# Optimization experiments

Hardware: AMD Instinct MI355X
Metric: run time of the kernel (lower is better)

## Reference

```python
import jax, jax.numpy as jnp
import numpy as np

B, S, DIN, DOUT = 4, 2048, 4096, 4096
W_SCALE = 64.0   # makes round(weight*scale) produce non-trivial int8 values
X_SCALE = 16.0   # input_scale so x*scale truncates to non-zero int32 values


def setup_inputs() -> dict:
    key = jax.random.key(0)
    k1, k2, k3 = jax.random.split(key, 3)
    # kaiming_uniform fan_in: bound = sqrt(6/fan_in)
    bound = float(np.sqrt(6.0 / DIN))
    weight = jax.random.uniform(k1, (DOUT, DIN), jnp.float32, -bound, bound)
    x = jax.random.normal(k2, (B, S, DIN), jnp.float32)
    bias = jax.random.normal(k3, (DOUT,), jnp.float32) * 0.01
    weight_scale = jnp.full((DOUT,), W_SCALE, jnp.float32)
    input_scale = jnp.full((1,), X_SCALE, jnp.float32)
    return {"x": x, "weight": weight, "bias": bias,
            "weight_scale": weight_scale, "input_scale": input_scale}


def reference(x, weight, bias, weight_scale, input_scale):
    # x = x * input_scale (pre-scale path of forward)
    xs = x * input_scale
    # fake-quant weights: round to int8 with wraparound, like torch .to(int8)
    w_int = jnp.round(weight * weight_scale[:, None]).astype(jnp.int8)
    # x.to(torch.int32): truncation toward zero
    x_int = xs.astype(jnp.int32)
    # F.linear on the integer-valued tensors (computed in f32: values are exact ints)
    acc = jnp.einsum('bsd,od->bso', x_int.astype(jnp.float32),
                     w_int.astype(jnp.float32))
    acc = acc + bias  # bias added inside linear
    # dequant: divide by per-channel weight_scale and the scalar input_scale
    out = acc / (weight_scale * input_scale)
    return out
```

## Files before the change

kernel.cpp:

```cpp
#include <hip/hip_runtime.h>

#define GM 8192
#define GN 4096
#define GK 4096

#define BM 128
#define BN 256
#define BK 64

using int4v = __attribute__((ext_vector_type(4))) int;

__global__ __launch_bounds__(256) void quant_x_k(const float4* __restrict__ x,
                                                 unsigned int* __restrict__ xq,
                                                 const float* __restrict__ iscale,
                                                 int n4) {
    int i = blockIdx.x * blockDim.x + threadIdx.x;
    if (i >= n4) return;
    float s = *iscale;
    float4 v = x[i];
    int q0 = (int)(v.x * s);
    int q1 = (int)(v.y * s);
    int q2 = (int)(v.z * s);
    int q3 = (int)(v.w * s);
    unsigned int packed = (unsigned int)(q0 & 0xff)
                        | ((unsigned int)(q1 & 0xff) << 8)
                        | ((unsigned int)(q2 & 0xff) << 16)
                        | ((unsigned int)(q3 & 0xff) << 24);
    xq[i] = packed;
}

__global__ __launch_bounds__(256) void quant_w_k(const float4* __restrict__ w,
                                                 unsigned int* __restrict__ wq,
                                                 const float* __restrict__ wscale,
                                                 int n4) {
    int i = blockIdx.x * blockDim.x + threadIdx.x;
    if (i >= n4) return;
    int row = i >> 10;
    float s = wscale[row];
    float4 v = w[i];
    int q0 = (int)rintf(v.x * s);
    int q1 = (int)rintf(v.y * s);
    int q2 = (int)rintf(v.z * s);
    int q3 = (int)rintf(v.w * s);
    unsigned int packed = (unsigned int)(q0 & 0xff)
                        | ((unsigned int)(q1 & 0xff) << 8)
                        | ((unsigned int)(q2 & 0xff) << 16)
                        | ((unsigned int)(q3 & 0xff) << 24);
    wq[i] = packed;
}

__global__ __launch_bounds__(256, 2) void qlinear_gemm_i8(
    const signed char* __restrict__ Aq,
    const signed char* __restrict__ Bq,
    const float* __restrict__ bias,
    const float* __restrict__ wscale,
    const float* __restrict__ iscale,
    float* __restrict__ C) {
    __shared__ signed char As[BM * BK];
    __shared__ signed char Bs[BN * BK];

    const int tid  = threadIdx.x;
    const int wave = tid >> 6;
    const int lane = tid & 63;
    const int m0 = blockIdx.x * BM;
    const int n0 = blockIdx.y * BN;
    const int wm = (wave >> 1) * 64;
    const int wn = (wave & 1) * 128;

    int4v acc[4][8];
#pragma unroll
    for (int i = 0; i < 4; ++i)
#pragma unroll
        for (int j = 0; j < 8; ++j)
            acc[i][j] = int4v{0, 0, 0, 0};

    const int kcl = (((lane & 3) ^ ((lane >> 3) & 3))) * 16;

    const int segA = wave * 2;
    const signed char* gA0 = Aq + (size_t)(m0 + segA * 16 + (lane >> 2)) * GK + kcl;
    signed char* lA0 = As + segA * 1024 + lane * 16;
    const int segB = wave * 4;
    const signed char* gB0 = Bq + (size_t)(n0 + segB * 16 + (lane >> 2)) * GK + kcl;
    signed char* lB0 = Bs + segB * 1024 + lane * 16;

    const int pos = ((lane >> 4) ^ ((lane >> 1) & 3)) * 16;
    const signed char* fA = As + (wm + (lane & 15)) * BK + pos;
    const signed char* fB = Bs + (wn + (lane & 15)) * BK + pos;

#define GLL16(g, l)                                                     \
    __builtin_amdgcn_global_load_lds(                                   \
        (__attribute__((address_space(1))) void*)(void*)(g),            \
        (__attribute__((address_space(3))) void*)(l), 16, 0, 0)

    for (int k0 = 0; k0 < GK; k0 += BK) {
        GLL16(gA0 + k0, lA0);
        GLL16(gA0 + (size_t)16 * GK + k0, lA0 + 1024);
        GLL16(gB0 + k0, lB0);
        GLL16(gB0 + (size_t)16 * GK + k0, lB0 + 1024);
        GLL16(gB0 + (size_t)32 * GK + k0, lB0 + 2048);
        GLL16(gB0 + (size_t)48 * GK + k0, lB0 + 3072);
        __syncthreads();

        int4v a[4], b[8];
#pragma unroll
        for (int i = 0; i < 4; ++i)
            a[i] = *(const int4v*)(fA + i * 16 * BK);
#pragma unroll
        for (int j = 0; j < 8; ++j)
            b[j] = *(const int4v*)(fB + j * 16 * BK);
#pragma unroll
        for (int mi = 0; mi < 4; ++mi)
#pragma unroll
            for (int ni = 0; ni < 8; ++ni)
                acc[mi][ni] = __builtin_amdgcn_mfma_i32_16x16x64_i8(
                    a[mi], b[ni], acc[mi][ni], 0, 0, 0);
        __syncthreads();
    }

    const float isc = *iscale;
#pragma unroll
    for (int ni = 0; ni < 8; ++ni) {
        const int col = n0 + wn + ni * 16 + (lane & 15);
        const float bs = bias[col];
        const float inv = 1.0f / (wscale[col] * isc);
#pragma unroll
        for (int mi = 0; mi < 4; ++mi) {
            const int row0 = m0 + wm + mi * 16 + (lane >> 4) * 4;
#pragma unroll
            for (int r = 0; r < 4; ++r) {
                C[(size_t)(row0 + r) * GN + col] =
                    ((float)acc[mi][ni][r] + bs) * inv;
            }
        }
    }
#undef GLL16
}

extern "C" void kernel_launch(void* const* d_in, const int* in_sizes, int n_in,
                              void* d_out, int out_size, void* d_ws, size_t ws_size,
                              hipStream_t stream) {
    const float* x      = (const float*)d_in[0];
    const float* w      = (const float*)d_in[1];
    const float* bias   = (const float*)d_in[2];
    const float* wscale = (const float*)d_in[3];
    const float* iscale = (const float*)d_in[4];
    float* out = (float*)d_out;

    signed char* xq = (signed char*)d_ws;
    signed char* wq = xq + (size_t)GM * GK;

    const int n4x = GM * GK / 4;
    quant_x_k<<<n4x / 256, 256, 0, stream>>>((const float4*)x,
                                             (unsigned int*)xq, iscale, n4x);
    const int n4w = GN * GK / 4;
    quant_w_k<<<n4w / 256, 256, 0, stream>>>((const float4*)w,
                                             (unsigned int*)wq, wscale, n4w);

    dim3 grid(GM / BM, GN / BN);
    qlinear_gemm_i8<<<grid, 256, 0, stream>>>(xq, wq, bias, wscale, iscale, out);
}
```

Measured before the change: 404.4 us.

## Double-buffer LDS tiles in int8 GEMM and fuse quantization kernels

The GEMM main loop now keeps two LDS buffers. It issues the global-to-LDS loads for the next K tile before running the MFMAs on the current one, so load latency can overlap compute instead of stalling at a barrier each iteration. The two quantization kernels are merged into one launch, and each thread now handles 16 elements with 16-byte stores. The trade-off is double the LDS use per block (48 KB), which could limit occupancy.

```diff
diff --git a/kernel.cpp b/kernel.cpp
--- a/kernel.cpp
+++ b/kernel.cpp
@@ -10,43 +10,43 @@
 
 using int4v = __attribute__((ext_vector_type(4))) int;
 
-__global__ __launch_bounds__(256) void quant_x_k(const float4* __restrict__ x,
-                                                 unsigned int* __restrict__ xq,
-                                                 const float* __restrict__ iscale,
-                                                 int n4) {
-    int i = blockIdx.x * blockDim.x + threadIdx.x;
-    if (i >= n4) return;
-    float s = *iscale;
-    float4 v = x[i];
-    int q0 = (int)(v.x * s);
-    int q1 = (int)(v.y * s);
-    int q2 = (int)(v.z * s);
-    int q3 = (int)(v.w * s);
-    unsigned int packed = (unsigned int)(q0 & 0xff)
-                        | ((unsigned int)(q1 & 0xff) << 8)
-                        | ((unsigned int)(q2 & 0xff) << 16)
-                        | ((unsigned int)(q3 & 0xff) << 24);
-    xq[i] = packed;
-}
-
-__global__ __launch_bounds__(256) void quant_w_k(const float4* __restrict__ w,
-                                                 unsigned int* __restrict__ wq,
-                                                 const float* __restrict__ wscale,
-                                                 int n4) {
-    int i = blockIdx.x * blockDim.x + threadIdx.x;
-    if (i >= n4) return;
-    int row = i >> 10;
-    float s = wscale[row];
-    float4 v = w[i];
-    int q0 = (int)rintf(v.x * s);
-    int q1 = (int)rintf(v.y * s);
-    int q2 = (int)rintf(v.z * s);
-    int q3 = (int)rintf(v.w * s);
-    unsigned int packed = (unsigned int)(q0 & 0xff)
-                        | ((unsigned int)(q1 & 0xff) << 8)
-                        | ((unsigned int)(q2 & 0xff) << 16)
-                        | ((unsigned int)(q3 & 0xff) << 24);
-    wq[i] = packed;
+__global__ __launch_bounds__(256) void quant_both(
+    const float4* __restrict__ x, uint4* __restrict__ xq,
+    const float4* __restrict__ w, uint4* __restrict__ wq,
+    const float* __restrict__ wscale, const float* __restrict__ iscale) {
+    const int b = blockIdx.x;
+    if (b < 8192) {
+        const float s = *iscale;
+        const int i = b * 256 + threadIdx.x;
+        unsigned int q[4];
+#pragma unroll
+        for (int j = 0; j < 4; ++j) {
+            float4 v = x[i * 4 + j];
+            int q0 = (int)(v.x * s);
+            int q1 = (int)(v.y * s);
+            int q2 = (int)(v.z * s);
+            int q3 = (int)(v.w * s);
+            q[j] = (unsigned int)(q0 & 0xff) | ((unsigned int)(q1 & 0xff) << 8)
+                 | ((unsigned int)(q2 & 0xff) << 16) | ((unsigned int)(q3 & 0xff) << 24);
+        }
+        xq[i] = uint4{q[0], q[1], q[2], q[3]};
+    } else {
+        const int row = b - 8192;
+        const float s = wscale[row];
+        const int i = row * 256 + threadIdx.x;
+        unsigned int q[4];
+#pragma unroll
+        for (int j = 0; j < 4; ++j) {
+            float4 v = w[i * 4 + j];
+            int q0 = (int)rintf(v.x * s);
+            int q1 = (int)rintf(v.y * s);
+            int q2 = (int)rintf(v.z * s);
+            int q3 = (int)rintf(v.w * s);
+            q[j] = (unsigned int)(q0 & 0xff) | ((unsigned int)(q1 & 0xff) << 8)
+                 | ((unsigned int)(q2 & 0xff) << 16) | ((unsigned int)(q3 & 0xff) << 24);
+        }
+        wq[i] = uint4{q[0], q[1], q[2], q[3]};
+    }
 }
 
 __global__ __launch_bounds__(256, 2) void qlinear_gemm_i8(
@@ -56,8 +56,8 @@
     const float* __restrict__ wscale,
     const float* __restrict__ iscale,
     float* __restrict__ C) {
-    __shared__ signed char As[BM * BK];
-    __shared__ signed char Bs[BN * BK];
+    __shared__ signed char As[2][BM * BK];
+    __shared__ signed char Bs[2][BN * BK];
 
     const int tid  = threadIdx.x;
     const int wave = tid >> 6;
@@ -74,33 +74,43 @@
         for (int j = 0; j < 8; ++j)
             acc[i][j] = int4v{0, 0, 0, 0};
 
-    const int kcl = (((lane & 3) ^ ((lane >> 3) & 3))) * 16;
-
+    const int kcl = ((lane & 3) ^ ((lane >> 3) & 3)) * 16;
     const int segA = wave * 2;
-    const signed char* gA0 = Aq + (size_t)(m0 + segA * 16 + (lane >> 2)) * GK + kcl;
-    signed char* lA0 = As + segA * 1024 + lane * 16;
+    const signed char* gA = Aq + (size_t)(m0 + segA * 16 + (lane >> 2)) * GK + kcl;
+    const int ldsA = segA * 1024 + lane * 16;
     const int segB = wave * 4;
-    const signed char* gB0 = Bq + (size_t)(n0 + segB * 16 + (lane >> 2)) * GK + kcl;
-    signed char* lB0 = Bs + segB * 1024 + lane * 16;
+    const signed char* gB = Bq + (size_t)(n0 + segB * 16 + (lane >> 2)) * GK + kcl;
+    const int ldsB = segB * 1024 + lane * 16;
 
     const int pos = ((lane >> 4) ^ ((lane >> 1) & 3)) * 16;
-    const signed char* fA = As + (wm + (lane & 15)) * BK + pos;
-    const signed char* fB = Bs + (wn + (lane & 15)) * BK + pos;
+    const int fAo = (wm + (lane & 15)) * BK + pos;
+    const int fBo = (wn + (lane & 15)) * BK + pos;
 
 #define GLL16(g, l)                                                     \
     __builtin_amdgcn_global_load_lds(                                   \
         (__attribute__((address_space(1))) void*)(void*)(g),            \
         (__attribute__((address_space(3))) void*)(l), 16, 0, 0)
 
+#define STAGE(buf, k)                                                   \
+    do {                                                                \
+        GLL16(gA + (k), &As[buf][ldsA]);                                \
+        GLL16(gA + (size_t)16 * GK + (k), &As[buf][ldsA + 1024]);       \
+        GLL16(gB + (k), &Bs[buf][ldsB]);                                \
+        GLL16(gB + (size_t)16 * GK + (k), &Bs[buf][ldsB + 1024]);       \
+        GLL16(gB + (size_t)32 * GK + (k), &Bs[buf][ldsB + 2048]);       \
+        GLL16(gB + (size_t)48 * GK + (k), &Bs[buf][ldsB + 3072]);       \
+    } while (0)
+
+    STAGE(0, 0);
+    __syncthreads();
+
     for (int k0 = 0; k0 < GK; k0 += BK) {
-        GLL16(gA0 + k0, lA0);
-        GLL16(gA0 + (size_t)16 * GK + k0, lA0 + 1024);
-        GLL16(gB0 + k0, lB0);
-        GLL16(gB0 + (size_t)16 * GK + k0, lB0 + 1024);
-        GLL16(gB0 + (size_t)32 * GK + k0, lB0 + 2048);
-        GLL16(gB0 + (size_t)48 * GK + k0, lB0 + 3072);
-        __syncthreads();
+        const int cur = (k0 >> 6) & 1;
+        const int nxt = cur ^ 1;
+        if (k0 + BK < GK) STAGE(nxt, k0 + BK);
 
+        const signed char* fA = &As[cur][fAo];
+        const signed char* fB = &Bs[cur][fBo];
         int4v a[4], b[8];
 #pragma unroll
         for (int i = 0; i < 4; ++i)
@@ -133,6 +143,7 @@
             }
         }
     }
+#undef STAGE
 #undef GLL16
 }
 
@@ -149,12 +160,9 @@
     signed char* xq = (signed char*)d_ws;
     signed char* wq = xq + (size_t)GM * GK;
 
-    const int n4x = GM * GK / 4;
-    quant_x_k<<<n4x / 256, 256, 0, stream>>>((const float4*)x,
-                                             (unsigned int*)xq, iscale, n4x);
-    const int n4w = GN * GK / 4;
-    quant_w_k<<<n4w / 256, 256, 0, stream>>>((const float4*)w,
-                                             (unsigned int*)wq, wscale, n4w);
+    quant_both<<<12288, 256, 0, stream>>>((const float4*)x, (uint4*)xq,
+                                          (const float4*)w, (uint4*)wq,
+                                          wscale, iscale);
 
     dim3 grid(GM / BM, GN / BN);
     qlinear_gemm_i8<<<grid, 256, 0, stream>>>(xq, wq, bias, wscale, iscale, out);
```

Result: no change. 407.4 us (+0.7%).
